# Optimization experiments

Hardware: AMD Instinct MI355X
Metric: run time of the kernel (lower is better)

The kernel has to match this reference:

```python
import jax, jax.numpy as jnp
import numpy as np

N_MEL = 80
PRENET = 256
ENC = 512
ARNN = 1024
DRNN = 1024
ATT = 128
NF = 32
K = 31
B, S, T = 16, 256, 400


def _lstm_cell(x, h, c, Wih, Whh, bih, bhh):
    # torch nn.LSTMCell math: gates ordered i, f, g, o
    z = x @ Wih.T + bih + h @ Whh.T + bhh
    i, f, g, o = jnp.split(z, 4, axis=-1)
    c_new = jax.nn.sigmoid(f) * c + jax.nn.sigmoid(i) * jnp.tanh(g)
    h_new = jax.nn.sigmoid(o) * jnp.tanh(c_new)
    return h_new, c_new


def setup_inputs() -> dict:
    key = jax.random.key(0)
    ks = jax.random.split(key, 24)
    g = lambda i, shape: (jax.random.normal(ks[i], shape, jnp.float32) * 0.02)
    inp = {
        'memory': jax.random.normal(ks[0], (B, S, ENC), jnp.float32),
        'decoder_inputs': jax.random.normal(ks[1], (B, N_MEL, T), jnp.float32),
        # prenet (LinearNorm, no bias in tacotron2 prenet)
        'Wpre1': g(2, (PRENET, N_MEL)),
        'Wpre2': g(3, (PRENET, PRENET)),
        # attention LSTMCell: input = prenet + enc = 256 + 512 = 768
        'Wih_a': g(4, (4 * ARNN, PRENET + ENC)),
        'Whh_a': g(5, (4 * ARNN, ARNN)),
        'bih_a': jnp.zeros((4 * ARNN,), jnp.float32),
        'bhh_a': jnp.zeros((4 * ARNN,), jnp.float32),
        # location-sensitive attention
        'Wq': g(6, (ATT, ARNN)),
        'Wm': g(7, (ATT, ENC)),
        'v': g(8, (ATT,)),
        'Wloc_conv': g(9, (NF, 2, K)),
        'Wloc_dense': g(10, (ATT, NF)),
        # decoder LSTMCell: input = att_rnn + enc = 1024 + 512 = 1536
        'Wih_d': g(11, (4 * DRNN, ARNN + ENC)),
        'Whh_d': g(12, (4 * DRNN, DRNN)),
        'bih_d': jnp.zeros((4 * DRNN,), jnp.float32),
        'bhh_d': jnp.zeros((4 * DRNN,), jnp.float32),
        # projections from [decoder_hidden ; context] = 1536
        'Wproj': g(13, (N_MEL, DRNN + ENC)),
        'bproj': jnp.zeros((N_MEL,), jnp.float32),
        'Wgate': g(14, (1, DRNN + ENC)),
        'bgate': jnp.zeros((1,), jnp.float32),
        'memory_lengths': jax.random.randint(ks[15], (B,), S // 2, S + 1),
    }
    return inp


def reference(memory, decoder_inputs, Wpre1, Wpre2, Wih_a, Whh_a, bih_a, bhh_a,
              Wq, Wm, v, Wloc_conv, Wloc_dense, Wih_d, Whh_d, bih_d, bhh_d,
              Wproj, bproj, Wgate, bgate, memory_lengths):
    # pad mask: True where position is beyond the encoder length
    pad_mask = jnp.arange(S)[None, :] >= memory_lengths[:, None]  # [B,S]
    proc_mem = memory @ Wm.T  # [B,S,ATT], memory_layer precomputed once

    # parse_decoder_inputs + go frame: [B,80,T] -> [T,B,80], prepend zeros
    di = jnp.transpose(decoder_inputs, (2, 0, 1))
    di = jnp.concatenate([jnp.zeros((1, B, N_MEL), di.dtype), di], axis=0)
    # prenet (dropout treated as identity for deterministic reference)
    pre = jax.nn.relu(jax.nn.relu(di @ Wpre1.T) @ Wpre2.T)  # [T+1,B,256]
    xs = pre[:-1]  # loop consumes indices 0..T-1

    carry0 = (jnp.zeros((B, ARNN)), jnp.zeros((B, ARNN)),
              jnp.zeros((B, DRNN)), jnp.zeros((B, DRNN)),
              jnp.zeros((B, S)), jnp.zeros((B, S)), jnp.zeros((B, ENC)))

    def step(carry, x):
        ah, ac, dh, dc, aw, awc, ctx = carry
        ah, ac = _lstm_cell(jnp.concatenate([x, ctx], -1), ah, ac,
                            Wih_a, Whh_a, bih_a, bhh_a)
        # location features from [prev_weights ; cum_weights]
        awcat = jnp.stack([aw, awc], axis=1)  # [B,2,S]
        loc = jax.lax.conv_general_dilated(
            awcat, Wloc_conv, (1,), ((K // 2, K // 2),),
            dimension_numbers=('NCH', 'OIH', 'NCH'))  # [B,NF,S]
        proc_att = jnp.einsum('bfs,af->bsa', loc, Wloc_dense)  # [B,S,ATT]
        q = ah @ Wq.T  # [B,ATT]
        e = jnp.tanh(q[:, None, :] + proc_att + proc_mem) @ v  # [B,S]
        e = jnp.where(pad_mask, -1e9, e)
        aw = jax.nn.softmax(e, axis=-1)
        ctx = jnp.einsum('bs,bse->be', aw, memory)  # [B,ENC]
        awc = awc + aw
        dh, dc = _lstm_cell(jnp.concatenate([ah, ctx], -1), dh, dc,
                            Wih_d, Whh_d, bih_d, bhh_d)
        hac = jnp.concatenate([dh, ctx], -1)  # [B,1536]
        mel = hac @ Wproj.T + bproj  # [B,80]
        gate = (hac @ Wgate.T + bgate)[:, 0]  # [B]
        return (ah, ac, dh, dc, aw, awc, ctx), (mel, gate, aw)

    _, (mels, gates, aligns) = jax.lax.scan(step, carry0, xs)
    mel_outputs = jnp.transpose(mels, (1, 2, 0))  # [B,80,T]
    gate_outputs = gates.T  # [B,T]
    alignments = jnp.transpose(aligns, (1, 0, 2))  # [B,T,S]
    return mel_outputs, gate_outputs, alignments
```

## Files before the change

### kernel.cpp

```cpp
#include <hip/hip_runtime.h>

typedef unsigned short ushort_t;
typedef unsigned int uint_t;
typedef float f32x4_t __attribute__((ext_vector_type(4)));
typedef short bf16x8_t __attribute__((ext_vector_type(8)));

#define NBATCH 16
#define SMEM   256
#define TSTEPS 400

#define F_XSB   0u
#define F_PM    819200u
#define F_MMIX  1343488u
#define F_W1T   1675264u
#define F_W2T   1695744u
#define F_AHB   1761280u
#define F_DHB   1777664u
#define F_CTXB  1794048u
#define F_DHF   1802240u
#define F_AWG   1835008u
#define F_FLG   1851392u
#define ZERO_BASE  F_AHB
#define ZERO_COUNT 95616u

#define AHF  0
#define CTXF 64
#define DHFL 192
#define AWF  320
#define PRF  336

#define A_AH    0
#define A_CTX   32768
#define A_XS    49152
#define A_RED   57344
#define D_AH    0
#define D_CTX   32768
#define D_DH    49152
#define D_MEMU  81920
#define D_COMB  114688
#define D_AWSM  120832
#define D_PART  121856
#define T_AH    0
#define T_LOCU  32768
#define T_QSM   53248
#define T_VSM   53760
#define T_ESM   54272
#define T_RED   55296
#define T_SMAW  55424
#define T_SMAWC 56448
#define P_DHP   0
#define P_AWP   65536
#define SMEM_BYTES 123904

struct Ptrs {
  const float *memory, *dec_in, *Wpre1, *Wpre2, *Wih_a, *Whh_a, *bih_a, *bhh_a,
              *Wq, *Wm, *v, *Wc, *Wld, *Wih_d, *Whh_d, *bih_d, *bhh_d,
              *Wproj, *bproj, *Wgate, *bgate;
  const int *mlen;
  float *ws;
  float *out;
};

__device__ __forceinline__ float ftanh(float x) {
  float e = __expf(2.f * x);
  return 1.f - 2.f / (e + 1.f);
}
__device__ __forceinline__ float fsig(float x) { return 1.f / (1.f + __expf(-x)); }

__device__ __forceinline__ unsigned f2bfbits(float x) {
  unsigned u = __builtin_bit_cast(unsigned, x);
  return (u + 0x7FFFu + ((u >> 16) & 1u)) >> 16;
}
__device__ __forceinline__ float bf2f(ushort_t u) {
  unsigned v = ((unsigned)u) << 16;
  return __builtin_bit_cast(float, v);
}
__device__ __forceinline__ bf16x8_t packbf8(const float* f) {
  bf16x8_t r;
#pragma unroll
  for (int j = 0; j < 8; ++j) r[j] = (short)f2bfbits(f[j]);
  return r;
}
__device__ __forceinline__ bf16x8_t pack_from_f4(const float* src) {
  const float4* s4 = (const float4*)src;
  float4 lo = s4[0], hi = s4[1];
  float tmp[8] = {lo.x, lo.y, lo.z, lo.w, hi.x, hi.y, hi.z, hi.w};
  return packbf8(tmp);
}
__device__ __forceinline__ bf16x8_t ldbf8(const ushort_t* p) {
  return *(const bf16x8_t*)p;
}
__device__ __forceinline__ unsigned long long ldull_a(const unsigned long long* p) {
  return __hip_atomic_load(p, __ATOMIC_RELAXED, __HIP_MEMORY_SCOPE_AGENT);
// ... 105 lines not shown
#pragma unroll
  for (int j = 0; j < 8; ++j) acc[j] = 0.f;
  for (int k = 0; k < 128; ++k) {
    float4 w = wm[k];
#pragma unroll
    for (int j = 0; j < 8; ++j) {
      float4 m = ((const float4*)(msl + (size_t)(sg * 8 + j) * 512))[k];
      acc[j] += w.x * m.x + w.y * m.y + w.z * m.z + w.w * m.w;
    }
  }
#pragma unroll
  for (int j = 0; j < 8; ++j)
    pm[((size_t)(b * SMEM + s0 + sg * 8 + j)) * 128 + a] = acc[j];
}

__global__ __launch_bounds__(512) void k_premix(Ptrs p) {
  const int b = blockIdx.x, tid = threadIdx.x;
  float* M = p.ws + F_MMIX;
  for (int i = tid; i < 81 * 256; i += 512) {
    int row = i >> 8, s = i & 255;
    const float* wrow = (row < 80) ? p.Wproj + (size_t)row * 1536 + 1024 : p.Wgate + 1024;
    const float4* w4 = (const float4*)wrow;
    const float4* m4 = (const float4*)(p.memory + ((size_t)(b * 256 + s)) * 512);
    float acc = 0.f;
#pragma unroll 4
    for (int k = 0; k < 128; ++k) {
      float4 w = w4[k], m = m4[k];
      acc += w.x * m.x + w.y * m.y + w.z * m.z + w.w * m.w;
    }
    M[((size_t)b * 81 + row) * 256 + s] = acc;
  }
}

__global__ __launch_bounds__(512, 1) void k_scan(Ptrs p) {
  extern __shared__ char smc[];
  const int bid = blockIdx.x, tid = threadIdx.x;
  const int wid = tid >> 6, lane = tid & 63;
  const int m16 = lane & 15, kq = lane >> 4;

  float* ws = p.ws;
  ushort_t* xsbU  = (ushort_t*)(ws + F_XSB);
  float*    pmF   = ws + F_PM;
  float*    Mx    = ws + F_MMIX;
  unsigned long long* ahb8 = (unsigned long long*)(ws + F_AHB);
  unsigned long long* dhb8 = (unsigned long long*)(ws + F_DHB);
  unsigned long long* ctxb8 = (unsigned long long*)(ws + F_CTXB);
  float*    dhfF  = ws + F_DHF;
  float*    awGF  = ws + F_AWG;
  int*      flg   = (int*)(ws + F_FLG);
  float* out_mel  = p.out;
  float* out_gate = p.out + 512000;
  float* out_al   = p.out + 518400;

  if (bid < 64) {
    const int ls = wid >> 1, half = wid & 1;
    const int strip = (bid << 2) | ls;
    const int gA = m16 & 3, jA = m16 >> 2;
    const int wrowA = gA * 1024 + strip * 4 + jA;
    bf16x8_t wA[28];
#pragma unroll
    for (int c = 0; c < 28; ++c) {
      int k0 = (half * 28 + c) * 32 + kq * 8;
      const float* src = (k0 < 768) ? p.Wih_a + (size_t)wrowA * 768 + k0
                                    : p.Whh_a + (size_t)wrowA * 1024 + (k0 - 768);
      wA[c] = pack_from_f4(src);
    }
    const int nnA = strip * 4 + kq;
    float biasA[4];
#pragma unroll
    for (int r = 0; r < 4; ++r) biasA[r] = p.bih_a[r * 1024 + nnA] + p.bhh_a[r * 1024 + nnA];
    float acState = 0.f;
    float* ared = (float*)(smc + A_RED);
    __syncthreads();

    for (int t = 0; t < TSTEPS; ++t) {
      const int pc = t & 1, pp = (t + 1) & 1;
      if (tid < 64) pollge(flg, AHF + tid, t);
      else if (tid < 192) pollge(flg, CTXF + tid - 64, t);
      __syncthreads();

      {
        const unsigned long long* ag = ahb8 + (size_t)pp * 4096;
        const unsigned long long* cg = ctxb8 + (size_t)pp * 2048;
        const unsigned long long* xg = (const unsigned long long*)xsbU + (size_t)t * 1024;
        unsigned long long tA[8], tC[4], tX[2];
#pragma unroll
        for (int i = 0; i < 8; ++i) tA[i] = ldull_a(ag + tid + i * 512);
#pragma unroll
        for (int i = 0; i < 4; ++i) tC[i] = ldull_a(cg + tid + i * 512);
#pragma unroll
        for (int i = 0; i < 2; ++i) tX[i] = xg[tid + i * 512];
#pragma unroll
        for (int i = 0; i < 8; ++i) { int u = tid + i * 512; lds_st8(smc, A_AH, u >> 8, 11, (u & 255) * 8, tA[i]); }
#pragma unroll
        for (int i = 0; i < 4; ++i) { int u = tid + i * 512; lds_st8(smc, A_CTX, u >> 7, 10, (u & 127) * 8, tC[i]); }
#pragma unroll
        for (int i = 0; i < 2; ++i) { int u = tid + i * 512; lds_st8(smc, A_XS, u >> 6, 9, (u & 63) * 8, tX[i]); }
      }
      __syncthreads();

      f32x4_t a0 = {0,0,0,0}, a1 = {0,0,0,0};
      if (half == 0) {
#pragma unroll
        for (int c = 0; c < 28; ++c) {
          bf16x8_t bf;
          if (c < 8)       bf = lds_bf8(smc, A_XS,  m16, 9,  c * 64 + kq * 16);
          else if (c < 24) bf = lds_bf8(smc, A_CTX, m16, 10, (c - 8) * 64 + kq * 16);
          else             bf = lds_bf8(smc, A_AH,  m16, 11, (c - 24) * 64 + kq * 16);
          if (c & 1) a1 = MFMA16(wA[c], bf, a1); else a0 = MFMA16(wA[c], bf, a0);
        }
      } else {
#pragma unroll
        for (int c = 0; c < 28; ++c) {
          bf16x8_t bf = lds_bf8(smc, A_AH, m16, 11, (4 + c) * 64 + kq * 16);
          if (c & 1) a1 = MFMA16(wA[c], bf, a1); else a0 = MFMA16(wA[c], bf, a0);
        }
#pragma unroll
        for (int r = 0; r < 4; ++r) ared[((ls * 64 + lane) << 2) + r] = a0[r] + a1[r];
      }
      __syncthreads();
      if (half == 0) {
        float z[4];
#pragma unroll
        for (int r = 0; r < 4; ++r)
          z[r] = a0[r] + a1[r] + ared[((ls * 64 + lane) << 2) + r] + biasA[r];
        float cn = fsig(z[1]) * acState + fsig(z[0]) * ftanh(z[2]);
        acState = cn;
        float h = fsig(z[3]) * ftanh(cn);
        unsigned hb = f2bfbits(h);
        unsigned b0 = __shfl(hb, m16);
        unsigned b1 = __shfl(hb, m16 + 16);
        unsigned b2 = __shfl(hb, m16 + 32);
        unsigned b3 = __shfl(hb, m16 + 48);
        if (kq == 0) {
          unsigned long long u = (unsigned long long)(b0 | (b1 << 16))
                               | ((unsigned long long)(b2 | (b3 << 16)) << 32);
          stull_a(ahb8 + ((size_t)(pc * 16 + m16)) * 256 + strip, u);
        }
      }
      __syncthreads();
      if (tid == 0) sig(flg, AHF + bid, t + 1);
    }
  } else if (bid < 192) {
    const int ls = wid >> 2, qt = wid & 3;
    const int strip = ((bid - 64) << 1) | ls;
    const int gD = m16 & 3, jD = m16 >> 2;
    const int wrowD = gD * 1024 + strip * 4 + jD;
    bf16x8_t wD[20];
#pragma unroll
    for (int c = 0; c < 20; ++c) {
      int k0 = (qt * 20 + c) * 32 + kq * 8;
      const float* src = (k0 < 1536) ? p.Wih_d + (size_t)wrowD * 1536 + k0
                                     : p.Whh_d + (size_t)wrowD * 1024 + (k0 - 1536);
      wD[c] = pack_from_f4(src);
    }
    const int nnD = strip * 4 + kq;
    float biasD[4];
#pragma unroll
    for (int r = 0; r < 4; ++r) biasD[r] = p.bih_d[r * 1024 + nnD] + p.bhh_d[r * 1024 + nnD];
    float dcState = 0.f;

    const int cb = (bid - 64) >> 3, sl = (bid - 64) & 7;
    float* comb = (float*)(smc + D_COMB);
    float* awsm = (float*)(smc + D_AWSM);
    float* part = (float*)(smc + D_PART);
    ushort_t* memu = (ushort_t*)(smc + D_MEMU);
    for (int i = tid; i < 16384; i += 512) {
      int s = i >> 6, c = i & 63;
      memu[i] = (ushort_t)f2bfbits(p.memory[((size_t)cb * 256 + s) * 512 + sl * 64 + c]);
    }
    __syncthreads();

    for (int t = 0; t <= TSTEPS; ++t) {
      const int pc = t & 1, pw = (t + 1) & 1;
      if (t >= 1) {
        if (tid < 64) pollge(flg, AHF + tid, t);
        else if (tid < 192) pollge(flg, CTXF + tid - 64, t);
        else if (tid < 320) pollge(flg, DHFL + tid - 192, t - 1);
        else if (tid < 328) pollge(flg, PRF + tid - 320, t - 2);
        __syncthreads();

        {
          const unsigned long long* ag = ahb8 + (size_t)pw * 4096;
          const unsigned long long* cg = ctxb8 + (size_t)pw * 2048;
          const unsigned long long* dg = dhb8 + (size_t)pc * 4096;
          unsigned long long tA[8], tC[4], tD[8];
#pragma unroll
          for (int i = 0; i < 8; ++i) tA[i] = ldull_a(ag + tid + i * 512);
#pragma unroll
          for (int i = 0; i < 4; ++i) tC[i] = ldull_a(cg + tid + i * 512);
#pragma unroll
          for (int i = 0; i < 8; ++i) tD[i] = ldull_a(dg + tid + i * 512);
#pragma unroll
          for (int i = 0; i < 8; ++i) { int u = tid + i * 512; lds_st8(smc, D_AH, u >> 8, 11, (u & 255) * 8, tA[i]); }
#pragma unroll
          for (int i = 0; i < 4; ++i) { int u = tid + i * 512; lds_st8(smc, D_CTX, u >> 7, 10, (u & 127) * 8, tC[i]); }
#pragma unroll
          for (int i = 0; i < 8; ++i) { int u = tid + i * 512; lds_st8(smc, D_DH, u >> 8, 11, (u & 255) * 8, tD[i]); }
        }
        __syncthreads();

        f32x4_t a0 = {0,0,0,0}, a1 = {0,0,0,0};
#define DFRAG_AH(ch)  lds_bf8(smc, D_AH,  m16, 11, (ch) * 64 + kq * 16)
#define DFRAG_CTX(ch) lds_bf8(smc, D_CTX, m16, 10, (ch) * 64 + kq * 16)
#define DFRAG_DH(ch)  lds_bf8(smc, D_DH,  m16, 11, (ch) * 64 + kq * 16)
#define DMFMA(BF) { bf16x8_t bf = (BF); \
          if (c & 1) a1 = MFMA16(wD[c], bf, a1); else a0 = MFMA16(wD[c], bf, a0); }
        if (qt == 0) {
#pragma unroll
          for (int c = 0; c < 20; ++c) DMFMA(DFRAG_AH(c))
        } else if (qt == 1) {
#pragma unroll
          for (int c = 0; c < 20; ++c) { if (c < 12) DMFMA(DFRAG_AH(20 + c)) else DMFMA(DFRAG_CTX(c - 12)) }
        } else if (qt == 2) {
#pragma unroll
          for (int c = 0; c < 20; ++c) { if (c < 8) DMFMA(DFRAG_CTX(8 + c)) else DMFMA(DFRAG_DH(c - 8)) }
        } else {
#pragma unroll
          for (int c = 0; c < 20; ++c) DMFMA(DFRAG_DH(12 + c))
        }
#undef DMFMA
        if (qt != 0) {
#pragma unroll
          for (int r = 0; r < 4; ++r)
            comb[(((ls * 3 + qt - 1) * 64 + lane) << 2) + r] = a0[r] + a1[r];
        }
        __syncthreads();
        if (qt == 0) {
          float z[4];
#pragma unroll
          for (int r = 0; r < 4; ++r) {
            z[r] = a0[r] + a1[r] + biasD[r];
#pragma unroll
            for (int j = 0; j < 3; ++j) z[r] += comb[(((ls * 3 + j) * 64 + lane) << 2) + r];
          }
          float cn = fsig(z[1]) * dcState + fsig(z[0]) * ftanh(z[2]);
          dcState = cn;
          float h = fsig(z[3]) * ftanh(cn);
          stf_a(dhfF + (size_t)pw * 16384 + m16 * 1024 + nnD, h);
          unsigned hb = f2bfbits(h);
          unsigned b0 = __shfl(hb, m16);
          unsigned b1 = __shfl(hb, m16 + 16);
          unsigned b2 = __shfl(hb, m16 + 32);
          unsigned b3 = __shfl(hb, m16 + 48);
          if (kq == 0) {
            unsigned long long u = (unsigned long long)(b0 | (b1 << 16))
                                 | ((unsigned long long)(b2 | (b3 << 16)) << 32);
            stull_a(dhb8 + ((size_t)(pw * 16 + m16)) * 256 + strip, u);
          }
        }
        __syncthreads();
        if (tid == 0) sig(flg, DHFL + (bid - 64), t);
      }
      if (t < TSTEPS) {
        if (tid == 0) pollge(flg, AWF + cb, t + 1);
        __syncthreads();
        if (tid < 256) awsm[tid] = ldf_a(awGF + (size_t)(t & 3) * 4096 + cb * 256 + tid);
        __syncthreads();
        const int c = tid & 63, sg = tid >> 6;
        float acc = 0.f;
#pragma unroll 8
        for (int si = 0; si < 32; ++si) {
          int s = sg * 32 + si;
          acc = fmaf(awsm[s], bf2f(memu[s * 64 + c]), acc);
        }
        part[sg * 64 + c] = acc;
        __syncthreads();
        if (tid < 64) {
          float v = 0.f;
#pragma unroll
          for (int j = 0; j < 8; ++j) v += part[j * 64 + tid];
          unsigned vb = f2bfbits(v);
          int base = tid & ~3;
          unsigned c0 = __shfl(vb, base);
          unsigned c1 = __shfl(vb, base + 1);
          unsigned c2 = __shfl(vb, base + 2);
          unsigned c3 = __shfl(vb, base + 3);
          if ((tid & 3) == 0) {
            unsigned long long u = (unsigned long long)(c0 | (c1 << 16))
                                 | ((unsigned long long)(c2 | (c3 << 16)) << 32);
            stull_a(ctxb8 + ((size_t)(pc * 16 + cb)) * 128 + ((sl * 64 + tid) >> 2), u);
          }
        }
        __syncthreads();
        if (tid == 0) sig(flg, CTXF + (bid - 64), t + 1);
      }
    }
  } else if (bid < 208) {
    const int b = bid - 192;
    const int mlenb = p.mlen[b];
    ushort_t* locu = (ushort_t*)(smc + T_LOCU);
    float* qsm   = (float*)(smc + T_QSM);
    float* vsm   = (float*)(smc + T_VSM);
    float* esm   = (float*)(smc + T_ESM);
    float* red   = (float*)(smc + T_RED);
    float* smaw  = (float*)(smc + T_SMAW);
    float* smawc = (float*)(smc + T_SMAWC);
    const ushort_t* wqp = (const ushort_t*)(ws + F_W1T);

    bf16x8_t wLd[8];
#pragma unroll
    for (int at = 0; at < 8; ++at)
      wLd[at] = pack_from_f4(p.Wld + ((size_t)(at * 16 + m16)) * 32 + kq * 8);
    bf16x8_t wC[2][2];
#pragma unroll
    for (int ft = 0; ft < 2; ++ft)
#pragma unroll
      for (int ck = 0; ck < 2; ++ck) {
        float tmp[8];
#pragma unroll
        for (int jj = 0; jj < 8; ++jj) {
          int k2 = ck * 32 + kq * 8 + jj;
          float vv = 0.f;
          if (k2 < 62) { int ch = (k2 < 31) ? 0 : 1; int k = k2 - 31 * ch;
            vv = p.Wc[((size_t)(ft * 16 + m16) * 2 + ch) * 31 + k]; }
          tmp[jj] = vv;
        }
        wC[ft][ck] = packbf8(tmp);
      }
    uint_t pmreg[2][8][2];
#pragma unroll
    for (int u = 0; u < 2; ++u) {
      int sloc = (wid * 2 + u) * 16 + m16;
#pragma unroll
      for (int at = 0; at < 8; ++at)
#pragma unroll
        for (int rp = 0; rp < 2; ++rp) {
          const float* src = pmF + ((size_t)(b * 256 + sloc)) * 128 + at * 16 + kq * 4 + rp * 2;
          pmreg[u][at][rp] = f2bfbits(src[0]) | (f2bfbits(src[1]) << 16);
        }
    }
    if (tid < 128) vsm[tid] = p.v[tid];
    if (tid < 256) { smaw[tid] = 0.f; smawc[tid] = 0.f; }
    __syncthreads();

    for (int t = 0; t < TSTEPS; ++t) {
      const int pc = t & 1;
#pragma unroll
      for (int u = 0; u < 4; ++u) {
        int task = wid * 4 + u;
        int stile = task >> 1, ft = task & 1;
        int scol = stile * 16 + m16;
        f32x4_t acc = {0,0,0,0};
#pragma unroll
        for (int ck = 0; ck < 2; ++ck) {
          float tmp[8];
#pragma unroll
          for (int jj = 0; jj < 8; ++jj) {
            int k2 = ck * 32 + kq * 8 + jj;
            float vv = 0.f;
            if (k2 < 62) {
              int ch = (k2 < 31) ? 0 : 1; int k = k2 - 31 * ch;
              int sp = scol + k - 15;
              if (sp >= 0 && sp < 256) vv = (ch ? smawc : smaw)[sp];
            }
            tmp[jj] = vv;
          }
          acc = MFMA16(wC[ft][ck], packbf8(tmp), acc);
        }
#pragma unroll
        for (int r = 0; r < 4; ++r)
          locu[scol * 40 + ft * 16 + kq * 4 + r] = (ushort_t)f2bfbits(acc[r]);
      }
      if (tid < 64) pollge(flg, AHF + tid, t + 1);
      else if (tid < 72) pollge(flg, PRF + (tid - 64), t - 3);
      __syncthreads();
      {
        const unsigned long long* ag = ahb8 + (size_t)pc * 4096;
        unsigned long long tA[8];
#pragma unroll
        for (int i = 0; i < 8; ++i) tA[i] = ldull_a(ag + tid + i * 512);
#pragma unroll
        for (int i = 0; i < 8; ++i) { int u = tid + i * 512; lds_st8(smc, T_AH, u >> 8, 11, (u & 255) * 8, tA[i]); }
      }
      __syncthreads();
      {
        f32x4_t acc = {0,0,0,0};
#pragma unroll
        for (int c = 0; c < 32; ++c) {
          bf16x8_t wf = ldbf8(wqp + (((size_t)(wid * 32 + c)) * 64 + lane) * 8);
          bf16x8_t hf = lds_bf8(smc, T_AH, m16, 11, c * 64 + kq * 16);
          acc = MFMA16(wf, hf, acc);
        }
        if (m16 == b) {
#pragma unroll
          for (int r = 0; r < 4; ++r) qsm[wid * 16 + kq * 4 + r] = acc[r];
        }
      }
      __syncthreads();
#pragma unroll
      for (int u = 0; u < 2; ++u) {
        int sloc = (wid * 2 + u) * 16 + m16;
        bf16x8_t Bfrag = ldbf8(locu + sloc * 40 + kq * 8);
        float eacc = 0.f;
#pragma unroll
        for (int at = 0; at < 8; ++at) {
          f32x4_t C = {0,0,0,0};
          C = MFMA16(wLd[at], Bfrag, C);
// ... 7 lines not shown
        }
        eacc += __shfl_xor(eacc, 16);
        eacc += __shfl_xor(eacc, 32);
        if (sloc >= mlenb) eacc = -1.0e9f;
        if (kq == 0) esm[sloc] = eacc;
      }
      __syncthreads();
      float ev = 0.f;
      if (tid < 256) {
        ev = esm[tid];
        float mv = ev;
        for (int o = 32; o; o >>= 1) mv = fmaxf(mv, __shfl_xor(mv, o));
        if (lane == 0) red[wid] = mv;
      }
      __syncthreads();
      float gmax = fmaxf(fmaxf(red[0], red[1]), fmaxf(red[2], red[3]));
      float pv = 0.f;
      if (tid < 256) {
        pv = __expf(ev - gmax);
        float sv = pv;
        for (int o = 32; o; o >>= 1) sv += __shfl_xor(sv, o);
        if (lane == 0) red[8 + wid] = sv;
      }
      __syncthreads();
      float gsum = red[8] + red[9] + red[10] + red[11];
      float awv = 0.f;
      if (tid < 256) {
        awv = pv / gsum;
        smaw[tid] = awv;
        smawc[tid] += awv;
        stf_a(awGF + (size_t)(t & 3) * 4096 + b * 256 + tid, awv);
      }
      __syncthreads();
      if (tid == 0) sig(flg, AWF + b, t + 1);
      if (tid < 256) out_al[((size_t)b * 400 + t) * 256 + tid] = awv;
    }
  } else if (bid < 216) {
    const int wv = (bid - 208) * 8 + wid;
    int rows[2] = {wv * 2, wv * 2 + 1};
    float wdh[2][16], mreg[2][16][4], biasr[2];
#pragma unroll
    for (int rr = 0; rr < 2; ++rr) {
      int row = rows[rr];
      biasr[rr] = 0.f;
#pragma unroll
      for (int j = 0; j < 16; ++j) wdh[rr][j] = 0.f;
#pragma unroll
      for (int b2 = 0; b2 < 16; ++b2)
#pragma unroll
        for (int j = 0; j < 4; ++j) mreg[rr][b2][j] = 0.f;
      if (row <= 80) {
        const float* wsrc = (row < 80) ? p.Wproj + (size_t)row * 1536 : p.Wgate;
#pragma unroll
        for (int j = 0; j < 16; ++j) wdh[rr][j] = wsrc[lane + 64 * j];
        biasr[rr] = (row < 80) ? p.bproj[row] : p.bgate[0];
#pragma unroll
        for (int b2 = 0; b2 < 16; ++b2)
#pragma unroll
          for (int j = 0; j < 4; ++j)
            mreg[rr][b2][j] = Mx[((size_t)b2 * 81 + row) * 256 + lane + 64 * j];
      }
    }
    float* dhp = (float*)(smc + P_DHP);
    float* awp = (float*)(smc + P_AWP);
    __syncthreads();
    for (int t = 1; t <= TSTEPS; ++t) {
      const int pw = (t + 1) & 1;
// ... 15 lines not shown
      }
      __syncthreads();
      if (wv <= 40) {
        for (int b2 = 0; b2 < 16; ++b2) {
          float h[16];
#pragma unroll
          for (int j = 0; j < 16; ++j) h[j] = dhp[b2 * 1024 + lane + 64 * j];
#pragma unroll
          for (int rr = 0; rr < 2; ++rr) {
            if (rows[rr] > 80) continue;
            float d = 0.f;
#pragma unroll
            for (int j = 0; j < 16; ++j) d = fmaf(wdh[rr][j], h[j], d);
#pragma unroll
            for (int j = 0; j < 4; ++j) d = fmaf(mreg[rr][b2][j], awp[b2 * 256 + lane + 64 * j], d);
            for (int o = 32; o; o >>= 1) d += __shfl_xor(d, o);
            if (lane == 0) {
              d += biasr[rr];
              if (rows[rr] < 80) out_mel[((size_t)b2 * 80 + rows[rr]) * 400 + (t - 1)] = d;
              else out_gate[(size_t)b2 * 400 + (t - 1)] = d;
            }
          }
        }
      }
      __syncthreads();
      if (tid == 0) sig(flg, PRF + (bid - 208), t);
    }
  }
}

extern "C" void kernel_launch(void* const* d_in, const int* in_sizes, int n_in,
                              void* d_out, int out_size, void* d_ws, size_t ws_size,
                              hipStream_t stream) {
  (void)in_sizes; (void)n_in; (void)out_size; (void)ws_size;
  Ptrs p;
  p.memory = (const float*)d_in[0];
  p.dec_in = (const float*)d_in[1];
  p.Wpre1  = (const float*)d_in[2];
  p.Wpre2  = (const float*)d_in[3];
  p.Wih_a  = (const float*)d_in[4];
  p.Whh_a  = (const float*)d_in[5];
  p.bih_a  = (const float*)d_in[6];
  p.bhh_a  = (const float*)d_in[7];
  p.Wq     = (const float*)d_in[8];
  p.Wm     = (const float*)d_in[9];
  p.v      = (const float*)d_in[10];
  p.Wc     = (const float*)d_in[11];
  p.Wld    = (const float*)d_in[12];
  p.Wih_d  = (const float*)d_in[13];
  p.Whh_d  = (const float*)d_in[14];
  p.bih_d  = (const float*)d_in[15];
  p.bhh_d  = (const float*)d_in[16];
  p.Wproj  = (const float*)d_in[17];
  p.bproj  = (const float*)d_in[18];
  p.Wgate  = (const float*)d_in[19];
  p.bgate  = (const float*)d_in[20];
  p.mlen   = (const int*)d_in[21];
  p.ws  = (float*)d_ws;
  p.out = (float*)d_out;

  static bool attr_done = false;
  if (!attr_done) {
    hipFuncSetAttribute((const void*)k_scan,
                        hipFuncAttributeMaxDynamicSharedMemorySize, SMEM_BYTES);
    attr_done = true;
  }

  hipLaunchKernelGGL(k_zero,      dim3((ZERO_COUNT + 255) / 256), dim3(256), 0, stream, p);
  hipLaunchKernelGGL(k_transpose, dim3(336), dim3(256), 0, stream, p);
  hipLaunchKernelGGL(k_prenet,    dim3(400), dim3(256), 0, stream, p);
  hipLaunchKernelGGL(k_packwq,    dim3(64),  dim3(256), 0, stream, p);
  hipLaunchKernelGGL(k_procmem,   dim3(256), dim3(256), 0, stream, p);
  hipLaunchKernelGGL(k_premix,    dim3(16),  dim3(512), 0, stream, p);
  hipLaunchKernelGGL(k_scan,      dim3(256), dim3(512), SMEM_BYTES, stream, p);
}
```

Measured before the change: 8.788 ms.

## Fuse context computation into attention blocks via MFMA and split flag polling

The attention-weighted context sum over memory moves out of the decoder-LSTM blocks and into the per-batch attention blocks. There it is computed with bf16 MFMA, with memory fragments held in registers, and published together with the alignment flag. The decoder and attention-LSTM blocks now poll the context flags separately, after loading the other operands, so those loads overlap the wait. This removes one cross-block handoff (attention weights to decoder blocks and back to context) from the serial per-step critical path. In exchange each attention block carries a large register load and extra per-step work, and the flag dependencies change.

```diff
diff --git a/kernel.cpp b/kernel.cpp
--- a/kernel.cpp
+++ b/kernel.cpp
@@ -36,10 +36,7 @@
 #define D_AH    0
 #define D_CTX   32768
 #define D_DH    49152
-#define D_MEMU  81920
 #define D_COMB  114688
-#define D_AWSM  120832
-#define D_PART  121856
 #define T_AH    0
 #define T_LOCU  32768
 #define T_QSM   53248
@@ -48,6 +45,7 @@
 #define T_RED   55296
 #define T_SMAW  55424
 #define T_SMAWC 56448
+#define T_CSM   57472
 #define P_DHP   0
 #define P_AWP   65536
 #define SMEM_BYTES 123904
@@ -274,26 +272,30 @@
     for (int t = 0; t < TSTEPS; ++t) {
       const int pc = t & 1, pp = (t + 1) & 1;
       if (tid < 64) pollge(flg, AHF + tid, t);
-      else if (tid < 192) pollge(flg, CTXF + tid - 64, t);
-      __syncthreads();
-
+      else if (tid >= 80 && tid < 208) pollge(flg, DHFL + (tid - 80), t - 1);
+      __syncthreads();
       {
         const unsigned long long* ag = ahb8 + (size_t)pp * 4096;
+        const unsigned long long* xg = (const unsigned long long*)xsbU + (size_t)t * 1024;
+        unsigned long long tA[8], tX[2];
+#pragma unroll
+        for (int i = 0; i < 8; ++i) tA[i] = ldull_a(ag + tid + i * 512);
+#pragma unroll
+        for (int i = 0; i < 2; ++i) tX[i] = xg[tid + i * 512];
+#pragma unroll
+        for (int i = 0; i < 8; ++i) { int u = tid + i * 512; lds_st8(smc, A_AH, u >> 8, 11, (u & 255) * 8, tA[i]); }
+#pragma unroll
+        for (int i = 0; i < 2; ++i) { int u = tid + i * 512; lds_st8(smc, A_XS, u >> 6, 9, (u & 63) * 8, tX[i]); }
+      }
+      if (tid >= 64 && tid < 80) pollge(flg, CTXF + (tid - 64), t);
+      __syncthreads();
+      {
         const unsigned long long* cg = ctxb8 + (size_t)pp * 2048;
-        const unsigned long long* xg = (const unsigned long long*)xsbU + (size_t)t * 1024;
-        unsigned long long tA[8], tC[4], tX[2];
-#pragma unroll
-        for (int i = 0; i < 8; ++i) tA[i] = ldull_a(ag + tid + i * 512);
+        unsigned long long tC[4];
 #pragma unroll
         for (int i = 0; i < 4; ++i) tC[i] = ldull_a(cg + tid + i * 512);
 #pragma unroll
-        for (int i = 0; i < 2; ++i) tX[i] = xg[tid + i * 512];
-#pragma unroll
-        for (int i = 0; i < 8; ++i) { int u = tid + i * 512; lds_st8(smc, A_AH, u >> 8, 11, (u & 255) * 8, tA[i]); }
-#pragma unroll
         for (int i = 0; i < 4; ++i) { int u = tid + i * 512; lds_st8(smc, A_CTX, u >> 7, 10, (u & 127) * 8, tC[i]); }
-#pragma unroll
-        for (int i = 0; i < 2; ++i) { int u = tid + i * 512; lds_st8(smc, A_XS, u >> 6, 9, (u & 63) * 8, tX[i]); }
       }
       __syncthreads();
 
@@ -357,132 +359,91 @@
 #pragma unroll
     for (int r = 0; r < 4; ++r) biasD[r] = p.bih_d[r * 1024 + nnD] + p.bhh_d[r * 1024 + nnD];
     float dcState = 0.f;
-
-    const int cb = (bid - 64) >> 3, sl = (bid - 64) & 7;
     float* comb = (float*)(smc + D_COMB);
-    float* awsm = (float*)(smc + D_AWSM);
-    float* part = (float*)(smc + D_PART);
-    ushort_t* memu = (ushort_t*)(smc + D_MEMU);
-    for (int i = tid; i < 16384; i += 512) {
-      int s = i >> 6, c = i & 63;
-      memu[i] = (ushort_t)f2bfbits(p.memory[((size_t)cb * 256 + s) * 512 + sl * 64 + c]);
-    }
     __syncthreads();
 
-    for (int t = 0; t <= TSTEPS; ++t) {
+    for (int t = 1; t <= TSTEPS; ++t) {
       const int pc = t & 1, pw = (t + 1) & 1;
-      if (t >= 1) {
-        if (tid < 64) pollge(flg, AHF + tid, t);
-        else if (tid < 192) pollge(flg, CTXF + tid - 64, t);
-        else if (tid < 320) pollge(flg, DHFL + tid - 192, t - 1);
-        else if (tid < 328) pollge(flg, PRF + tid - 320, t - 2);
-        __syncthreads();
-
-        {
-          const unsigned long long* ag = ahb8 + (size_t)pw * 4096;
-          const unsigned long long* cg = ctxb8 + (size_t)pw * 2048;
-          const unsigned long long* dg = dhb8 + (size_t)pc * 4096;
-          unsigned long long tA[8], tC[4], tD[8];
-#pragma unroll
-          for (int i = 0; i < 8; ++i) tA[i] = ldull_a(ag + tid + i * 512);
-#pragma unroll
-          for (int i = 0; i < 4; ++i) tC[i] = ldull_a(cg + tid + i * 512);
-#pragma unroll
-          for (int i = 0; i < 8; ++i) tD[i] = ldull_a(dg + tid + i * 512);
-#pragma unroll
-          for (int i = 0; i < 8; ++i) { int u = tid + i * 512; lds_st8(smc, D_AH, u >> 8, 11, (u & 255) * 8, tA[i]); }
-#pragma unroll
-          for (int i = 0; i < 4; ++i) { int u = tid + i * 512; lds_st8(smc, D_CTX, u >> 7, 10, (u & 127) * 8, tC[i]); }
-#pragma unroll
-          for (int i = 0; i < 8; ++i) { int u = tid + i * 512; lds_st8(smc, D_DH, u >> 8, 11, (u & 255) * 8, tD[i]); }
-        }
-        __syncthreads();
-
-        f32x4_t a0 = {0,0,0,0}, a1 = {0,0,0,0};
+      if (tid < 64) pollge(flg, AHF + tid, t);
+      else if (tid >= 80 && tid < 208) pollge(flg, DHFL + (tid - 80), t - 1);
+      else if (tid >= 208 && tid < 216) pollge(flg, PRF + (tid - 208), t - 2);
+      __syncthreads();
+      {
+        const unsigned long long* ag = ahb8 + (size_t)pw * 4096;
+        const unsigned long long* dg = dhb8 + (size_t)pc * 4096;
+        unsigned long long tA[8], tD[8];
+#pragma unroll
+        for (int i = 0; i < 8; ++i) tA[i] = ldull_a(ag + tid + i * 512);
+#pragma unroll
+        for (int i = 0; i < 8; ++i) tD[i] = ldull_a(dg + tid + i * 512);
+#pragma unroll
+        for (int i = 0; i < 8; ++i) { int u = tid + i * 512; lds_st8(smc, D_AH, u >> 8, 11, (u & 255) * 8, tA[i]); }
+#pragma unroll
+        for (int i = 0; i < 8; ++i) { int u = tid + i * 512; lds_st8(smc, D_DH, u >> 8, 11, (u & 255) * 8, tD[i]); }
+      }
+      if (tid >= 64 && tid < 80) pollge(flg, CTXF + (tid - 64), t);
+      __syncthreads();
+      {
+        const unsigned long long* cg = ctxb8 + (size_t)pw * 2048;
+        unsigned long long tC[4];
+#pragma unroll
+        for (int i = 0; i < 4; ++i) tC[i] = ldull_a(cg + tid + i * 512);
+#pragma unroll
+        for (int i = 0; i < 4; ++i) { int u = tid + i * 512; lds_st8(smc, D_CTX, u >> 7, 10, (u & 127) * 8, tC[i]); }
+      }
+      __syncthreads();
+
+      f32x4_t a0 = {0,0,0,0}, a1 = {0,0,0,0};
 #define DFRAG_AH(ch)  lds_bf8(smc, D_AH,  m16, 11, (ch) * 64 + kq * 16)
 #define DFRAG_CTX(ch) lds_bf8(smc, D_CTX, m16, 10, (ch) * 64 + kq * 16)
 #define DFRAG_DH(ch)  lds_bf8(smc, D_DH,  m16, 11, (ch) * 64 + kq * 16)
 #define DMFMA(BF) { bf16x8_t bf = (BF); \
-          if (c & 1) a1 = MFMA16(wD[c], bf, a1); else a0 = MFMA16(wD[c], bf, a0); }
-        if (qt == 0) {
-#pragma unroll
-          for (int c = 0; c < 20; ++c) DMFMA(DFRAG_AH(c))
-        } else if (qt == 1) {
-#pragma unroll
-          for (int c = 0; c < 20; ++c) { if (c < 12) DMFMA(DFRAG_AH(20 + c)) else DMFMA(DFRAG_CTX(c - 12)) }
-        } else if (qt == 2) {
-#pragma unroll
-          for (int c = 0; c < 20; ++c) { if (c < 8) DMFMA(DFRAG_CTX(8 + c)) else DMFMA(DFRAG_DH(c - 8)) }
-        } else {
-#pragma unroll
-          for (int c = 0; c < 20; ++c) DMFMA(DFRAG_DH(12 + c))
-        }
+        if (c & 1) a1 = MFMA16(wD[c], bf, a1); else a0 = MFMA16(wD[c], bf, a0); }
+      if (qt == 0) {
+#pragma unroll
+        for (int c = 0; c < 20; ++c) DMFMA(DFRAG_AH(c))
+      } else if (qt == 1) {
+#pragma unroll
+        for (int c = 0; c < 20; ++c) { if (c < 12) DMFMA(DFRAG_AH(20 + c)) else DMFMA(DFRAG_CTX(c - 12)) }
+      } else if (qt == 2) {
+#pragma unroll
+        for (int c = 0; c < 20; ++c) { if (c < 8) DMFMA(DFRAG_CTX(8 + c)) else DMFMA(DFRAG_DH(c - 8)) }
+      } else {
+#pragma unroll
+        for (int c = 0; c < 20; ++c) DMFMA(DFRAG_DH(12 + c))
+      }
 #undef DMFMA
-        if (qt != 0) {
-#pragma unroll
-          for (int r = 0; r < 4; ++r)
-            comb[(((ls * 3 + qt - 1) * 64 + lane) << 2) + r] = a0[r] + a1[r];
-        }
-        __syncthreads();
-        if (qt == 0) {
-          float z[4];
-#pragma unroll
-          for (int r = 0; r < 4; ++r) {
-            z[r] = a0[r] + a1[r] + biasD[r];
-#pragma unroll
-            for (int j = 0; j < 3; ++j) z[r] += comb[(((ls * 3 + j) * 64 + lane) << 2) + r];
-          }
-          float cn = fsig(z[1]) * dcState + fsig(z[0]) * ftanh(z[2]);
-          dcState = cn;
-          float h = fsig(z[3]) * ftanh(cn);
-          stf_a(dhfF + (size_t)pw * 16384 + m16 * 1024 + nnD, h);
-          unsigned hb = f2bfbits(h);
-          unsigned b0 = __shfl(hb, m16);
-          unsigned b1 = __shfl(hb, m16 + 16);
-          unsigned b2 = __shfl(hb, m16 + 32);
-          unsigned b3 = __shfl(hb, m16 + 48);
-          if (kq == 0) {
-            unsigned long long u = (unsigned long long)(b0 | (b1 << 16))
-                                 | ((unsigned long long)(b2 | (b3 << 16)) << 32);
-            stull_a(dhb8 + ((size_t)(pw * 16 + m16)) * 256 + strip, u);
-          }
-        }
-        __syncthreads();
-        if (tid == 0) sig(flg, DHFL + (bid - 64), t);
-      }
-      if (t < TSTEPS) {
-        if (tid == 0) pollge(flg, AWF + cb, t + 1);
-        __syncthreads();
-        if (tid < 256) awsm[tid] = ldf_a(awGF + (size_t)(t & 3) * 4096 + cb * 256 + tid);
-        __syncthreads();
-        const int c = tid & 63, sg = tid >> 6;
-        float acc = 0.f;
-#pragma unroll 8
-        for (int si = 0; si < 32; ++si) {
-          int s = sg * 32 + si;
-          acc = fmaf(awsm[s], bf2f(memu[s * 64 + c]), acc);
-        }
-        part[sg * 64 + c] = acc;
-        __syncthreads();
-        if (tid < 64) {
-          float v = 0.f;
-#pragma unroll
-          for (int j = 0; j < 8; ++j) v += part[j * 64 + tid];
-          unsigned vb = f2bfbits(v);
-          int base = tid & ~3;
-          unsigned c0 = __shfl(vb, base);
-          unsigned c1 = __shfl(vb, base + 1);
-          unsigned c2 = __shfl(vb, base + 2);
-          unsigned c3 = __shfl(vb, base + 3);
-          if ((tid & 3) == 0) {
-            unsigned long long u = (unsigned long long)(c0 | (c1 << 16))
-                                 | ((unsigned long long)(c2 | (c3 << 16)) << 32);
-            stull_a(ctxb8 + ((size_t)(pc * 16 + cb)) * 128 + ((sl * 64 + tid) >> 2), u);
-          }
-        }
-        __syncthreads();
-        if (tid == 0) sig(flg, CTXF + (bid - 64), t + 1);
-      }
+      if (qt != 0) {
+#pragma unroll
+        for (int r = 0; r < 4; ++r)
+          comb[(((ls * 3 + qt - 1) * 64 + lane) << 2) + r] = a0[r] + a1[r];
+      }
+      __syncthreads();
+      if (qt == 0) {
+        float z[4];
+#pragma unroll
+        for (int r = 0; r < 4; ++r) {
+          z[r] = a0[r] + a1[r] + biasD[r];
+#pragma unroll
+          for (int j = 0; j < 3; ++j) z[r] += comb[(((ls * 3 + j) * 64 + lane) << 2) + r];
+        }
+        float cn = fsig(z[1]) * dcState + fsig(z[0]) * ftanh(z[2]);
+        dcState = cn;
+        float h = fsig(z[3]) * ftanh(cn);
+        stf_a(dhfF + (size_t)pw * 16384 + m16 * 1024 + nnD, h);
+        unsigned hb = f2bfbits(h);
+        unsigned b0 = __shfl(hb, m16);
+        unsigned b1 = __shfl(hb, m16 + 16);
+        unsigned b2 = __shfl(hb, m16 + 32);
+        unsigned b3 = __shfl(hb, m16 + 48);
+        if (kq == 0) {
+          unsigned long long u = (unsigned long long)(b0 | (b1 << 16))
+                               | ((unsigned long long)(b2 | (b3 << 16)) << 32);
+          stull_a(dhb8 + ((size_t)(pw * 16 + m16)) * 256 + strip, u);
+        }
+      }
+      __syncthreads();
+      if (tid == 0) sig(flg, DHFL + (bid - 64), t);
     }
   } else if (bid < 208) {
     const int b = bid - 192;
@@ -494,6 +455,7 @@
     float* red   = (float*)(smc + T_RED);
     float* smaw  = (float*)(smc + T_SMAW);
     float* smawc = (float*)(smc + T_SMAWC);
+    float* csm   = (float*)(smc + T_CSM);
     const ushort_t* wqp = (const ushort_t*)(ws + F_W1T);
 
     bf16x8_t wLd[8];
@@ -527,6 +489,19 @@
           const float* src = pmF + ((size_t)(b * 256 + sloc)) * 128 + at * 16 + kq * 4 + rp * 2;
           pmreg[u][at][rp] = f2bfbits(src[0]) | (f2bfbits(src[1]) << 16);
         }
+    }
+    bf16x8_t memfr[4][8];
+#pragma unroll
+    for (int u = 0; u < 4; ++u) {
+      int c = (wid * 4 + u) * 16 + m16;
+#pragma unroll
+      for (int kc = 0; kc < 8; ++kc) {
+        float tmp[8];
+#pragma unroll
+        for (int j = 0; j < 8; ++j)
+          tmp[j] = p.memory[((size_t)b * 256 + kc * 32 + kq * 8 + j) * 512 + c];
+        memfr[u][kc] = packbf8(tmp);
+      }
     }
     if (tid < 128) vsm[tid] = p.v[tid];
     if (tid < 256) { smaw[tid] = 0.f; smawc[tid] = 0.f; }
@@ -561,7 +536,8 @@
           locu[scol * 40 + ft * 16 + kq * 4 + r] = (ushort_t)f2bfbits(acc[r]);
       }
       if (tid < 64) pollge(flg, AHF + tid, t + 1);
-      else if (tid < 72) pollge(flg, PRF + (tid - 64), t - 3);
+      else if (tid >= 80 && tid < 208) pollge(flg, DHFL + (tid - 80), t - 1);
+      else if (tid >= 208 && tid < 216) pollge(flg, PRF + (tid - 208), t - 2);
       __syncthreads();
       {
         const unsigned long long* ag = ahb8 + (size_t)pc * 4096;
@@ -635,7 +611,38 @@
         stf_a(awGF + (size_t)(t & 3) * 4096 + b * 256 + tid, awv);
       }
       __syncthreads();
-      if (tid == 0) sig(flg, AWF + b, t + 1);
+      {
+        f32x4_t c0 = {0,0,0,0}, c1 = {0,0,0,0}, c2 = {0,0,0,0}, c3 = {0,0,0,0};
+#pragma unroll
+        for (int kc = 0; kc < 8; ++kc) {
+          float awt[8];
+#pragma unroll
+          for (int j = 0; j < 8; ++j) awt[j] = smaw[kc * 32 + kq * 8 + j];
+          bf16x8_t awf = packbf8(awt);
+          c0 = MFMA16(memfr[0][kc], awf, c0);
+          c1 = MFMA16(memfr[1][kc], awf, c1);
+          c2 = MFMA16(memfr[2][kc], awf, c2);
+          c3 = MFMA16(memfr[3][kc], awf, c3);
+        }
+        if (m16 == 0) {
+#pragma unroll
+          for (int r = 0; r < 4; ++r) {
+            csm[(wid * 4 + 0) * 16 + kq * 4 + r] = c0[r];
+            csm[(wid * 4 + 1) * 16 + kq * 4 + r] = c1[r];
+            csm[(wid * 4 + 2) * 16 + kq * 4 + r] = c2[r];
+            csm[(wid * 4 + 3) * 16 + kq * 4 + r] = c3[r];
+          }
+        }
+      }
+      __syncthreads();
+      if (tid < 128) {
+        float c0 = csm[tid * 4], c1 = csm[tid * 4 + 1], c2 = csm[tid * 4 + 2], c3 = csm[tid * 4 + 3];
+        unsigned long long u = (unsigned long long)(f2bfbits(c0) | (f2bfbits(c1) << 16))
+                             | ((unsigned long long)(f2bfbits(c2) | (f2bfbits(c3) << 16)) << 32);
+        stull_a(ctxb8 + ((size_t)(pc * 16 + b)) * 128 + tid, u);
+      }
+      __syncthreads();
+      if (tid == 0) { sig(flg, AWF + b, t + 1); sig(flg, CTXF + b, t + 1); }
       if (tid < 256) out_al[((size_t)b * 400 + t) * 256 + tid] = awv;
     }
   } else if (bid < 216) {
```

New measurement: 11.17 ms. 1.27x slower.

## Precompute Wih_a·memory so attention LSTM reads alignment weights instead of context

Applied to the files above, without the earlier changes.

Adds a k_gmix pre-kernel that multiplies the context slice of Wih_a by memory for every batch and encoder position, stored as bf16 (G = Wctx·memory). The attention-LSTM blocks then form the context contribution as G·aw, using the previous step's alignment weights, so they no longer wait on the context vector and drop 8 MFMA chunks per wave. This breaks the dependency on the context-producing blocks and may shorten the per-step critical path. In exchange it adds a 4096x4096 GEMM up front, a 32 MB workspace buffer, and a 256-long scalar FMA dot product per thread each step. It is used only when the workspace is large enough.

```diff
diff --git a/kernel.cpp b/kernel.cpp
--- a/kernel.cpp
+++ b/kernel.cpp
@@ -22,6 +22,8 @@
 #define F_FLG   1851392u
 #define ZERO_BASE  F_AHB
 #define ZERO_COUNT 95616u
+#define F_G     1856896u
+#define WS_NEED_G ((size_t)(F_G + 8388608u) * 4u)
 
 #define AHF  0
 #define CTXF 64
@@ -33,6 +35,9 @@
 #define A_CTX   32768
 #define A_XS    49152
 #define A_RED   57344
+#define AG_AWP  32768
+#define AG_XS   49280
+#define AG_RED  57472
 #define D_AH    0
 #define D_CTX   32768
 #define D_DH    49152
@@ -59,6 +64,7 @@
   const int *mlen;
   float *ws;
   float *out;
+  int use_g;
 };
 
 __device__ __forceinline__ float ftanh(float x) {
@@ -230,6 +236,36 @@
   }
 }
 
+__global__ __launch_bounds__(256) void k_gmix(Ptrs p) {
+  const int tid = threadIdx.x, w = tid >> 6, lane = tid & 63;
+  const int m16 = lane & 15, kq = lane >> 4;
+  const int Mt = blockIdx.x >> 6, Nt = blockIdx.x & 63;
+  const int arow = Mt * 64 + w * 16 + m16;
+  f32x4_t acc[4];
+#pragma unroll
+  for (int nt = 0; nt < 4; ++nt) acc[nt] = (f32x4_t){0,0,0,0};
+  for (int kc = 0; kc < 16; ++kc) {
+    bf16x8_t af = pack_from_f4(p.Wih_a + (size_t)arow * 768 + 256 + kc * 32 + kq * 8);
+#pragma unroll
+    for (int nt = 0; nt < 4; ++nt) {
+      int n = Nt * 64 + nt * 16 + m16;
+      bf16x8_t bfr = pack_from_f4(p.memory + (size_t)n * 512 + kc * 32 + kq * 8);
+      acc[nt] = MFMA16(af, bfr, acc[nt]);
+    }
+  }
+  ushort_t* gp = (ushort_t*)(p.ws + F_G);
+#pragma unroll
+  for (int nt = 0; nt < 4; ++nt) {
+    int n = Nt * 64 + nt * 16 + m16;
+    int b = n >> 8, s = n & 255;
+#pragma unroll
+    for (int r = 0; r < 4; ++r) {
+      int R = Mt * 64 + w * 16 + kq * 4 + r;
+      gp[(size_t)R * 4096 + (s >> 3) * 128 + b * 8 + (s & 7)] = (ushort_t)f2bfbits(acc[nt][r]);
+    }
+  }
+}
+
 __global__ __launch_bounds__(512, 1) void k_scan(Ptrs p) {
   extern __shared__ char smc[];
   const int bid = blockIdx.x, tid = threadIdx.x;
@@ -255,89 +291,206 @@
     const int strip = (bid << 2) | ls;
     const int gA = m16 & 3, jA = m16 >> 2;
     const int wrowA = gA * 1024 + strip * 4 + jA;
-    bf16x8_t wA[28];
-#pragma unroll
-    for (int c = 0; c < 28; ++c) {
-      int k0 = (half * 28 + c) * 32 + kq * 8;
-      const float* src = (k0 < 768) ? p.Wih_a + (size_t)wrowA * 768 + k0
-                                    : p.Whh_a + (size_t)wrowA * 1024 + (k0 - 768);
-      wA[c] = pack_from_f4(src);
-    }
     const int nnA = strip * 4 + kq;
     float biasA[4];
 #pragma unroll
     for (int r = 0; r < 4; ++r) biasA[r] = p.bih_a[r * 1024 + nnA] + p.bhh_a[r * 1024 + nnA];
     float acState = 0.f;
-    float* ared = (float*)(smc + A_RED);
-    __syncthreads();
-
-    for (int t = 0; t < TSTEPS; ++t) {
-      const int pc = t & 1, pp = (t + 1) & 1;
-      if (tid < 64) pollge(flg, AHF + tid, t);
-      else if (tid < 192) pollge(flg, CTXF + tid - 64, t);
-      __syncthreads();
-
-      {
-        const unsigned long long* ag = ahb8 + (size_t)pp * 4096;
-        const unsigned long long* cg = ctxb8 + (size_t)pp * 2048;
-        const unsigned long long* xg = (const unsigned long long*)xsbU + (size_t)t * 1024;
-        unsigned long long tA[8], tC[4], tX[2];
-#pragma unroll
-        for (int i = 0; i < 8; ++i) tA[i] = ldull_a(ag + tid + i * 512);
-#pragma unroll
-        for (int i = 0; i < 4; ++i) tC[i] = ldull_a(cg + tid + i * 512);
-#pragma unroll
-        for (int i = 0; i < 2; ++i) tX[i] = xg[tid + i * 512];
-#pragma unroll
-        for (int i = 0; i < 8; ++i) { int u = tid + i * 512; lds_st8(smc, A_AH, u >> 8, 11, (u & 255) * 8, tA[i]); }
-#pragma unroll
-        for (int i = 0; i < 4; ++i) { int u = tid + i * 512; lds_st8(smc, A_CTX, u >> 7, 10, (u & 127) * 8, tC[i]); }
-#pragma unroll
-        for (int i = 0; i < 2; ++i) { int u = tid + i * 512; lds_st8(smc, A_XS, u >> 6, 9, (u & 63) * 8, tX[i]); }
-      }
-      __syncthreads();
-
-      f32x4_t a0 = {0,0,0,0}, a1 = {0,0,0,0};
-      if (half == 0) {
-#pragma unroll
-        for (int c = 0; c < 28; ++c) {
-          bf16x8_t bf;
-          if (c < 8)       bf = lds_bf8(smc, A_XS,  m16, 9,  c * 64 + kq * 16);
-          else if (c < 24) bf = lds_bf8(smc, A_CTX, m16, 10, (c - 8) * 64 + kq * 16);
-          else             bf = lds_bf8(smc, A_AH,  m16, 11, (c - 24) * 64 + kq * 16);
-          if (c & 1) a1 = MFMA16(wA[c], bf, a1); else a0 = MFMA16(wA[c], bf, a0);
-        }
-      } else {
-#pragma unroll
-        for (int c = 0; c < 28; ++c) {
-          bf16x8_t bf = lds_bf8(smc, A_AH, m16, 11, (4 + c) * 64 + kq * 16);
-          if (c & 1) a1 = MFMA16(wA[c], bf, a1); else a0 = MFMA16(wA[c], bf, a0);
-        }
-#pragma unroll
-        for (int r = 0; r < 4; ++r) ared[((ls * 64 + lane) << 2) + r] = a0[r] + a1[r];
-      }
-      __syncthreads();
-      if (half == 0) {
-        float z[4];
-#pragma unroll
-        for (int r = 0; r < 4; ++r)
-          z[r] = a0[r] + a1[r] + ared[((ls * 64 + lane) << 2) + r] + biasA[r];
-        float cn = fsig(z[1]) * acState + fsig(z[0]) * ftanh(z[2]);
-        acState = cn;
-        float h = fsig(z[3]) * ftanh(cn);
-        unsigned hb = f2bfbits(h);
-        unsigned b0 = __shfl(hb, m16);
-        unsigned b1 = __shfl(hb, m16 + 16);
-        unsigned b2 = __shfl(hb, m16 + 32);
-        unsigned b3 = __shfl(hb, m16 + 48);
-        if (kq == 0) {
-          unsigned long long u = (unsigned long long)(b0 | (b1 << 16))
-                               | ((unsigned long long)(b2 | (b3 << 16)) << 32);
-          stull_a(ahb8 + ((size_t)(pc * 16 + m16)) * 256 + strip, u);
-        }
-      }
-      __syncthreads();
-      if (tid == 0) sig(flg, AHF + bid, t + 1);
+
+    if (p.use_g) {
+      bf16x8_t wAg[20];
+#pragma unroll
+      for (int c = 0; c < 20; ++c) {
+        int cc = half * 20 + c;
+        const float* src = (cc < 8) ? p.Wih_a + (size_t)wrowA * 768 + cc * 32 + kq * 8
+                                    : p.Whh_a + (size_t)wrowA * 1024 + (cc - 8) * 32 + kq * 8;
+        wAg[c] = pack_from_f4(src);
+      }
+      float* ared = (float*)(smc + AG_RED);
+      float* awp  = (float*)(smc + AG_AWP);
+      const ushort_t* Gp = (const ushort_t*)(ws + F_G);
+      const ushort_t* g0p = Gp + ((size_t)((half * 2 + 0) * 1024 + strip * 4 + kq)) * 4096 + m16 * 8;
+      const ushort_t* g1p = Gp + ((size_t)((half * 2 + 1) * 1024 + strip * 4 + kq)) * 4096 + m16 * 8;
+      __syncthreads();
+
+      for (int t = 0; t < TSTEPS; ++t) {
+        const int pc = t & 1, pp = (t + 1) & 1;
+        if (tid < 64) pollge(flg, AHF + tid, t);
+        else if (tid >= 80 && tid < 208) pollge(flg, DHFL + (tid - 80), t - 1);
+        __syncthreads();
+        {
+          const unsigned long long* ag = ahb8 + (size_t)pp * 4096;
+          const unsigned long long* xg = (const unsigned long long*)xsbU + (size_t)t * 1024;
+          unsigned long long tA[8], tX[2];
+#pragma unroll
+          for (int i = 0; i < 8; ++i) tA[i] = ldull_a(ag + tid + i * 512);
+#pragma unroll
+          for (int i = 0; i < 2; ++i) tX[i] = xg[tid + i * 512];
+#pragma unroll
+          for (int i = 0; i < 8; ++i) { int u = tid + i * 512; lds_st8(smc, A_AH, u >> 8, 11, (u & 255) * 8, tA[i]); }
+#pragma unroll
+          for (int i = 0; i < 2; ++i) { int u = tid + i * 512; lds_st8(smc, AG_XS, u >> 6, 9, (u & 63) * 8, tX[i]); }
+        }
+        if (tid >= 64 && tid < 80) pollge(flg, AWF + (tid - 64), t);
+        __syncthreads();
+        {
+          const unsigned long long* ag8 = (const unsigned long long*)(awGF + (size_t)((t + 3) & 3) * 4096);
+          unsigned long long tw[4];
+#pragma unroll
+          for (int i = 0; i < 4; ++i) tw[i] = ldull_a(ag8 + tid + i * 512);
+#pragma unroll
+          for (int i = 0; i < 4; ++i) {
+            int u = (tid + i * 512) * 2;
+            int row = u >> 8, col = u & 255;
+            float2 f = __builtin_bit_cast(float2, tw[i]);
+            awp[row * 257 + col] = f.x;
+            awp[row * 257 + col + 1] = f.y;
+          }
+        }
+        __syncthreads();
+
+        float gd0 = 0.f, gd1 = 0.f;
+        {
+          const float* awrow = awp + m16 * 257;
+#pragma unroll 4
+          for (int sc = 0; sc < 32; ++sc) {
+            bf16x8_t ga = ldbf8(g0p + sc * 128);
+            bf16x8_t gb = ldbf8(g1p + sc * 128);
+#pragma unroll
+            for (int j = 0; j < 8; ++j) {
+              float av = awrow[sc * 8 + j];
+              gd0 = fmaf(bf2f((ushort_t)ga[j]), av, gd0);
+              gd1 = fmaf(bf2f((ushort_t)gb[j]), av, gd1);
+            }
+          }
+        }
+        f32x4_t a0 = {0,0,0,0}, a1 = {0,0,0,0};
+        if (half == 0) {
+#pragma unroll
+          for (int c = 0; c < 20; ++c) {
+            bf16x8_t bf = (c < 8) ? lds_bf8(smc, AG_XS, m16, 9, c * 64 + kq * 16)
+                                  : lds_bf8(smc, A_AH, m16, 11, (c - 8) * 64 + kq * 16);
+            if (c & 1) a1 = MFMA16(wAg[c], bf, a1); else a0 = MFMA16(wAg[c], bf, a0);
+          }
+        } else {
+#pragma unroll
+          for (int c = 0; c < 20; ++c) {
+            bf16x8_t bf = lds_bf8(smc, A_AH, m16, 11, (12 + c) * 64 + kq * 16);
+            if (c & 1) a1 = MFMA16(wAg[c], bf, a1); else a0 = MFMA16(wAg[c], bf, a0);
+          }
+#pragma unroll
+          for (int r = 0; r < 4; ++r) {
+            float e = a0[r] + a1[r];
+            if (r == 2) e += gd0;
+            if (r == 3) e += gd1;
+            ared[((ls * 64 + lane) << 2) + r] = e;
+          }
+        }
+        __syncthreads();
+        if (half == 0) {
+          float z[4];
+#pragma unroll
+          for (int r = 0; r < 4; ++r) {
+            z[r] = a0[r] + a1[r] + ared[((ls * 64 + lane) << 2) + r] + biasA[r];
+            if (r == 0) z[r] += gd0;
+            if (r == 1) z[r] += gd1;
+          }
+          float cn = fsig(z[1]) * acState + fsig(z[0]) * ftanh(z[2]);
+          acState = cn;
+          float h = fsig(z[3]) * ftanh(cn);
+          unsigned hb = f2bfbits(h);
+          unsigned b0 = __shfl(hb, m16);
+          unsigned b1 = __shfl(hb, m16 + 16);
+          unsigned b2 = __shfl(hb, m16 + 32);
+          unsigned b3 = __shfl(hb, m16 + 48);
+          if (kq == 0) {
+            unsigned long long u = (unsigned long long)(b0 | (b1 << 16))
+                                 | ((unsigned long long)(b2 | (b3 << 16)) << 32);
+            stull_a(ahb8 + ((size_t)(pc * 16 + m16)) * 256 + strip, u);
+          }
+        }
+        __syncthreads();
+        if (tid == 0) sig(flg, AHF + bid, t + 1);
+      }
+    } else {
+      bf16x8_t wA[28];
+#pragma unroll
+      for (int c = 0; c < 28; ++c) {
+        int k0 = (half * 28 + c) * 32 + kq * 8;
+        const float* src = (k0 < 768) ? p.Wih_a + (size_t)wrowA * 768 + k0
+                                      : p.Whh_a + (size_t)wrowA * 1024 + (k0 - 768);
+        wA[c] = pack_from_f4(src);
+      }
+      float* ared = (float*)(smc + A_RED);
+      __syncthreads();
+
+      for (int t = 0; t < TSTEPS; ++t) {
+        const int pc = t & 1, pp = (t + 1) & 1;
+        if (tid < 64) pollge(flg, AHF + tid, t);
+        else if (tid < 192) pollge(flg, CTXF + tid - 64, t);
+        __syncthreads();
+        {
+          const unsigned long long* ag = ahb8 + (size_t)pp * 4096;
+          const unsigned long long* cg = ctxb8 + (size_t)pp * 2048;
+          const unsigned long long* xg = (const unsigned long long*)xsbU + (size_t)t * 1024;
+          unsigned long long tA[8], tC[4], tX[2];
+#pragma unroll
+          for (int i = 0; i < 8; ++i) tA[i] = ldull_a(ag + tid + i * 512);
+#pragma unroll
+          for (int i = 0; i < 4; ++i) tC[i] = ldull_a(cg + tid + i * 512);
+#pragma unroll
+          for (int i = 0; i < 2; ++i) tX[i] = xg[tid + i * 512];
+#pragma unroll
+          for (int i = 0; i < 8; ++i) { int u = tid + i * 512; lds_st8(smc, A_AH, u >> 8, 11, (u & 255) * 8, tA[i]); }
+#pragma unroll
+          for (int i = 0; i < 4; ++i) { int u = tid + i * 512; lds_st8(smc, A_CTX, u >> 7, 10, (u & 127) * 8, tC[i]); }
+#pragma unroll
+          for (int i = 0; i < 2; ++i) { int u = tid + i * 512; lds_st8(smc, A_XS, u >> 6, 9, (u & 63) * 8, tX[i]); }
+        }
+        __syncthreads();
+
+        f32x4_t a0 = {0,0,0,0}, a1 = {0,0,0,0};
+        if (half == 0) {
+#pragma unroll
+          for (int c = 0; c < 28; ++c) {
+            bf16x8_t bf;
+            if (c < 8)       bf = lds_bf8(smc, A_XS,  m16, 9,  c * 64 + kq * 16);
+            else if (c < 24) bf = lds_bf8(smc, A_CTX, m16, 10, (c - 8) * 64 + kq * 16);
+            else             bf = lds_bf8(smc, A_AH,  m16, 11, (c - 24) * 64 + kq * 16);
+            if (c & 1) a1 = MFMA16(wA[c], bf, a1); else a0 = MFMA16(wA[c], bf, a0);
+          }
+        } else {
+#pragma unroll
+          for (int c = 0; c < 28; ++c) {
+            bf16x8_t bf = lds_bf8(smc, A_AH, m16, 11, (4 + c) * 64 + kq * 16);
+            if (c & 1) a1 = MFMA16(wA[c], bf, a1); else a0 = MFMA16(wA[c], bf, a0);
+          }
+#pragma unroll
+          for (int r = 0; r < 4; ++r) ared[((ls * 64 + lane) << 2) + r] = a0[r] + a1[r];
+        }
+        __syncthreads();
+        if (half == 0) {
+          float z[4];
+#pragma unroll
+          for (int r = 0; r < 4; ++r)
+            z[r] = a0[r] + a1[r] + ared[((ls * 64 + lane) << 2) + r] + biasA[r];
+          float cn = fsig(z[1]) * acState + fsig(z[0]) * ftanh(z[2]);
+          acState = cn;
+          float h = fsig(z[3]) * ftanh(cn);
+          unsigned hb = f2bfbits(h);
+          unsigned b0 = __shfl(hb, m16);
+          unsigned b1 = __shfl(hb, m16 + 16);
+          unsigned b2 = __shfl(hb, m16 + 32);
+          unsigned b3 = __shfl(hb, m16 + 48);
+          if (kq == 0) {
+            unsigned long long u = (unsigned long long)(b0 | (b1 << 16))
+                                 | ((unsigned long long)(b2 | (b3 << 16)) << 32);
+            stull_a(ahb8 + ((size_t)(pc * 16 + m16)) * 256 + strip, u);
+          }
+        }
+        __syncthreads();
+        if (tid == 0) sig(flg, AHF + bid, t + 1);
+      }
     }
   } else if (bid < 192) {
     const int ls = wid >> 2, qt = wid & 3;
@@ -717,7 +870,7 @@
 extern "C" void kernel_launch(void* const* d_in, const int* in_sizes, int n_in,
                               void* d_out, int out_size, void* d_ws, size_t ws_size,
                               hipStream_t stream) {
-  (void)in_sizes; (void)n_in; (void)out_size; (void)ws_size;
+  (void)in_sizes; (void)n_in; (void)out_size;
   Ptrs p;
   p.memory = (const float*)d_in[0];
   p.dec_in = (const float*)d_in[1];
@@ -743,6 +896,7 @@
   p.mlen   = (const int*)d_in[21];
   p.ws  = (float*)d_ws;
   p.out = (float*)d_out;
+  p.use_g = (ws_size >= WS_NEED_G) ? 1 : 0;
 
   static bool attr_done = false;
   if (!attr_done) {
@@ -757,5 +911,7 @@
   hipLaunchKernelGGL(k_packwq,    dim3(64),  dim3(256), 0, stream, p);
   hipLaunchKernelGGL(k_procmem,   dim3(256), dim3(256), 0, stream, p);
   hipLaunchKernelGGL(k_premix,    dim3(16),  dim3(512), 0, stream, p);
+  if (p.use_g)
+    hipLaunchKernelGGL(k_gmix,    dim3(4096), dim3(256), 0, stream, p);
   hipLaunchKernelGGL(k_scan,      dim3(256), dim3(512), SMEM_BYTES, stream, p);
 }
```

After: 15.37 ms. 1.75x slower.
